# Kernel tuning notes

Measured on AMD Instinct MI355X. Metric: run time of the kernel, lower is better.

Reference implementation:

```python
import jax, jax.numpy as jnp
import numpy as np

DIM = 256
HALF = DIM // 2
B, S = 32, 4096
U_MAX = 4096          # upper bound on number of unique tree positions (positions < S)
MAX_DEPTH = 13        # bitlen(S) covers all path lengths for positions <= S


def setup_inputs() -> dict:
    key = jax.random.key(0)
    k1, k2, k3, k4, k5 = jax.random.split(key, 5)
    token_types = jax.random.randint(k1, (B, S), 0, 5, dtype=jnp.int32)
    node_positions = jax.random.randint(k2, (B, S), 0, S, dtype=jnp.int32)
    small_vals = jax.random.randint(k3, (B, S), 0, 4, dtype=jnp.int32)
    # deBruijn tokens (type 4) reference tree positions -> values must lie in unique(node_positions)
    token_values = jnp.where(token_types == 4, node_positions,
                   jnp.where(token_types == 3, -1, small_vals)).astype(jnp.int32)
    primitives = jax.random.normal(k4, (2, HALF, HALF), dtype=jnp.float32)
    identity = jnp.ones((1, HALF), dtype=jnp.float32)
    embed_weight = jax.random.normal(k5, (11, HALF), dtype=jnp.float32)
    return {"token_types": token_types, "token_values": token_values,
            "node_positions": node_positions, "primitives": primitives,
            "identity": identity, "embed_weight": embed_weight}


def cayley(X):
    # torch orthogonal(..., orthogonal_map='cayley'): A = tril(X) - tril(X)^T (skew), Q = (I - A/2)^{-1}(I + A/2)
    A = jnp.tril(X)
    A = A - jnp.swapaxes(A, -1, -2)
    I = jnp.eye(X.shape[-1], dtype=X.dtype)
    return jnp.linalg.solve(I - 0.5 * A, I + 0.5 * A)


def _forward(token_types, token_values, node_positions, primitives, identity, embed_weight):
    Q = cayley(primitives)                                   # [2, h, h] orthogonal maps
    flat_pos = node_positions.ravel()
    uniq, inv = jnp.unique(flat_pos, return_inverse=True, size=U_MAX, fill_value=S)
    inv = inv.ravel()

    # binary path of pos: bit d of pos for d < bitlen(pos)-1, padded with 2 (pos<=1 -> empty path)
    d = jnp.arange(MAX_DEPTH, dtype=uniq.dtype)
    bits = (uniq[:, None] >> d) & 1                           # [U, D]
    valid = (uniq[:, None] >> (d + 1)) > 0
    word = jnp.where(valid, bits, 2)                          # [U, D]

    maps0 = jnp.broadcast_to(identity, (U_MAX, HALF)).astype(primitives.dtype)

    def step(maps, b):                                        # maps [U, h], b [U]
        m0 = maps @ Q[0].T                                    # linear(maps, primitives[0])
        m1 = maps @ Q[1].T
        maps = jnp.where((b == 0)[:, None], m0,
                jnp.where((b == 1)[:, None], m1, maps))
        return maps, None

    path_emb, _ = jax.lax.scan(step, maps0, word.T)           # [U, h]

    pos_enc = path_emb[inv].reshape(B, S, HALF)               # positional encodings

    sos = token_types == 0
    bop = token_types == 1
    nop = token_types == 2
    oos = (token_types == 3) & (token_values == -1)
    db = token_types == 4

    emb_idx = jnp.where(bop, token_values + 1,
              jnp.where(nop, token_values + 5, 0))
    type_emb = embed_weight[emb_idx]                          # [B, S, h]

    db_idx = jnp.searchsorted(uniq, jnp.clip(token_values, 0, S - 1))  # bucketize into unique positions
    db_emb = path_emb[db_idx]                                 # [B, S, h]

    content = jnp.zeros_like(pos_enc)
    content = jnp.where(sos[..., None], embed_weight[0], content)
    content = jnp.where((bop | nop)[..., None], type_emb, content)
    content = jnp.where(db[..., None], db_emb, content)
    content = jnp.where(oos[..., None], embed_weight[10], content)

    return jnp.concatenate([content, pos_enc], axis=-1)       # [B, S, DIM]


def reference(token_types, token_values, node_positions, primitives, identity, embed_weight):
    return _forward(token_types, token_values, node_positions, primitives, identity, embed_weight)
```

## Files before the change

### kernel.cpp

```cpp
#include <hip/hip_runtime.h>

#define HALF 128
#define NMAT 16384
#define NTOK 131072

typedef float f4 __attribute__((ext_vector_type(4)));

__device__ __forceinline__ float nval(const float* __restrict__ X, int r, int c) {
    int mx = r > c ? r : c;
    int mn = r ^ c ^ mx;
    float x = X[mx * HALF + mn];
    return (r == c) ? 1.0f : (r > c ? 0.5f * x : -0.5f * x);
}


template<int S, bool FIRST>
__global__ __launch_bounds__(256) void k1_panel(const float* __restrict__ prim,
                                                const float* __restrict__ W,
                                                float* __restrict__ RBws) {
    __shared__ __align__(16) float Rs[16][132];
    __shared__ float Dc[16][17];
    const int b  = blockIdx.x;
    const int t  = threadIdx.x;
    const int k0 = S << 4;
    const float* __restrict__ X  = prim + b * NMAT;
    const float* __restrict__ Wb = W + b * NMAT;

    {
        const int j  = t >> 4;
        const int c0 = (t & 15) << 3;
        if (FIRST) {
            #pragma unroll
            for (int u = 0; u < 8; ++u) Rs[j][c0 + u] = nval(X, k0 + j, c0 + u);
        } else {
            float4 a  = *(const float4*)&Wb[(k0 + j) * HALF + c0];
            float4 b2 = *(const float4*)&Wb[(k0 + j) * HALF + c0 + 4];
            *(float4*)&Rs[j][c0]     = a;
            *(float4*)&Rs[j][c0 + 4] = b2;
        }
    }
    __syncthreads();

    if (t < 64) {
        const int cp = t & 15, q4 = t >> 4;
        float dd[4];
        #pragma unroll
        for (int i = 0; i < 4; ++i) dd[i] = Rs[q4 * 4 + i][k0 + cp];
        #pragma unroll
        for (int k = 0; k < 16; ++k) {
            float cv[4];
            #pragma unroll
            for (int i = 0; i < 4; ++i) cv[i] = __shfl(dd[i], (q4 << 4) | k);
            float rv   = __shfl(dd[k & 3], ((k >> 2) << 4) | cp);
            float dkk  = __shfl(rv, k);
            float dinv = 1.0f / dkk;
            float sv   = rv * dinv;
            bool  own  = (cp == k);
            float rf   = own ? dinv : sv;
            #pragma unroll
            for (int i = 0; i < 4; ++i)
                dd[i] = own ? (-dd[i] * dinv) : fmaf(-cv[i], sv, dd[i]);
            dd[k & 3] = (q4 == (k >> 2)) ? rf : dd[k & 3];
        }
        #pragma unroll
        for (int i = 0; i < 4; ++i) Dc[cp][q4 * 4 + i] = dd[i];
    }
    __syncthreads();

    {
        const int m  = t >> 4;
        const int c0 = (t & 15) << 3;
        float* __restrict__ RBb = RBws + b * (16 * HALF);
        if (c0 == k0 || c0 == k0 + 8) {
            #pragma unroll
            for (int u = 0; u < 8; ++u) RBb[m * HALF + c0 + u] = Dc[c0 + u - k0][m];
        } else {
            float acc[8] = {0.f,0.f,0.f,0.f,0.f,0.f,0.f,0.f};
            #pragma unroll
            for (int j = 0; j < 16; ++j) {
                float dj = Dc[j][m];
                #pragma unroll
                for (int u = 0; u < 8; ++u)
                    acc[u] = fmaf(dj, Rs[j][c0 + u], acc[u]);
            }
            *(float4*)&RBb[m * HALF + c0]     = make_float4(acc[0], acc[1], acc[2], acc[3]);
            *(float4*)&RBb[m * HALF + c0 + 4] = make_float4(acc[4], acc[5], acc[6], acc[7]);
        }
    }
}

template<int S, bool FIRST, bool LAST>
__global__ __launch_bounds__(256) void k1_update(const float* __restrict__ prim,
                                                 float* __restrict__ W,
                                                 const float* __restrict__ RBws) {
    __shared__ __align__(16) float RBs[16][132];
    __shared__ float Cs[16][17];
    const int blk = blockIdx.x;
    const int b   = blk >> 3;
    const int rg  = blk & 7;
    const int r0  = rg << 4;
    const int t   = threadIdx.x;
    const int k0  = S << 4;
    const float* __restrict__ X   = prim + b * NMAT;
    float* __restrict__ Wb        = W + b * NMAT;
    const float* __restrict__ RBb = RBws + b * (16 * HALF);

    {
        const int m  = t >> 4;
        const int c0 = (t & 15) << 3;
        *(float4*)&RBs[m][c0]     = *(const float4*)&RBb[m * HALF + c0];
        *(float4*)&RBs[m][c0 + 4] = *(const float4*)&RBb[m * HALF + c0 + 4];
    }
    {
        const int rr = t >> 4, m = t & 15;
        Cs[rr][m] = FIRST ? nval(X, r0 + rr, k0 + m)
                          : Wb[(r0 + rr) * HALF + k0 + m];
    }
    __syncthreads();

    const int rr = t >> 4;
    const int r  = r0 + rr;
    const int c0 = (t & 15) << 3;
    float w[8];

    if (rg == S) {
        #pragma unroll
        for (int u = 0; u < 8; ++u) w[u] = RBs[rr][c0 + u];
    } else {
        const bool pan = (c0 == k0) || (c0 == k0 + 8);
        if (pan) {
            #pragma unroll
            for (int u = 0; u < 8; ++u) w[u] = 0.0f;
        } else if (FIRST) {
            #pragma unroll
            for (int u = 0; u < 8; ++u) w[u] = nval(X, r, c0 + u);
        } else {
            float4 a  = *(const float4*)&Wb[r * HALF + c0];
            float4 b2 = *(const float4*)&Wb[r * HALF + c0 + 4];
            w[0]=a.x; w[1]=a.y; w[2]=a.z; w[3]=a.w;
            w[4]=b2.x; w[5]=b2.y; w[6]=b2.z; w[7]=b2.w;
        }
        #pragma unroll
        for (int m = 0; m < 16; ++m) {
            float cm = Cs[rr][m];
            #pragma unroll
            for (int u = 0; u < 8; ++u)
                w[u] = fmaf(-cm, RBs[m][c0 + u], w[u]);
        }
    }

    if (LAST) {
        #pragma unroll
        for (int u = 0; u < 8; ++u)
            w[u] = 2.0f * w[u] - ((r == c0 + u) ? 1.0f : 0.0f);
    }
    *(float4*)&Wb[r * HALF + c0]     = make_float4(w[0], w[1], w[2], w[3]);
    *(float4*)&Wb[r * HALF + c0 + 4] = make_float4(w[4], w[5], w[6], w[7]);
}

__global__ __launch_bounds__(256) void path_base(const float* __restrict__ QT,
                                                 const float* __restrict__ ident,
                                                 float* __restrict__ P) {
    __shared__ __align__(16) float vs[2][4][HALF];
    const int t    = threadIdx.x;
    const int rg   = t >> 6;
    const int jj   = (t & 63) << 1;
    const int v    = (blockIdx.x << 2) + rg;
    const int vmax = (blockIdx.x << 2) + 3;

    float2 cv = *(const float2*)&ident[jj];
    *(float2*)&vs[0][rg][jj] = cv;
    __syncthreads();

    int cur = 0;
    for (int d = 0; d < 8; ++d) {
        if ((vmax >> (d + 1)) == 0) break;
        const bool valid = (v >> (d + 1)) > 0;
        const float* __restrict__ Qm = QT + (((v >> d) & 1) ? NMAT : 0);
        float2 acc = make_float2(0.f, 0.f);
        #pragma unroll 4
        for (int cc = 0; cc < 128; cc += 4) {
            float4 v4 = *(const float4*)&vs[cur][rg][cc];
            float2 q0 = *(const float2*)&Qm[(cc+0)*HALF + jj];
            float2 q1 = *(const float2*)&Qm[(cc+1)*HALF + jj];
            float2 q2 = *(const float2*)&Qm[(cc+2)*HALF + jj];
            float2 q3 = *(const float2*)&Qm[(cc+3)*HALF + jj];
            acc.x = fmaf(v4.x,q0.x, fmaf(v4.y,q1.x, fmaf(v4.z,q2.x, fmaf(v4.w,q3.x, acc.x))));
            acc.y = fmaf(v4.x,q0.y, fmaf(v4.y,q1.y, fmaf(v4.z,q2.y, fmaf(v4.w,q3.y, acc.y))));
        }
        if (valid) cv = acc;
        *(float2*)&vs[cur ^ 1][rg][jj] = cv;
        __syncthreads();
        cur ^= 1;
    }
    *(float2*)&P[v * HALF + jj] = cv;
}

__global__ __launch_bounds__(256) void path_upper(const float* __restrict__ QT,
                                                  float* __restrict__ P) {
    __shared__ __align__(16) float vs[2][8][HALF];
    const int t  = threadIdx.x;
    const int j  = t & 127;
    const int h  = t >> 7;
    const int k  = 2 + (blockIdx.x >> 4);
    const int r0 = (blockIdx.x & 15) << 3;

    float acc[4];
    #pragma unroll
    for (int rr = 0; rr < 4; ++rr)
        acc[rr] = P[(128 + r0 + h * 4 + rr) * HALF + j];

    int p = 0;
    for (int d = 7; d < 13; ++d) {
        if ((k >> (d - 6)) == 0) break;
        const float* __restrict__ Qm = QT + (((k >> (d - 7)) & 1) ? NMAT : 0);
        #pragma unroll
        for (int rr = 0; rr < 4; ++rr) vs[p][h * 4 + rr][j] = acc[rr];
        __syncthreads();

        float nacc[4] = {0.f, 0.f, 0.f, 0.f};
        #pragma unroll 4
        for (int cc = 0; cc < 128; cc += 4) {
            float q0 = Qm[(cc + 0) * HALF + j];
            float q1 = Qm[(cc + 1) * HALF + j];
            float q2 = Qm[(cc + 2) * HALF + j];
            float q3 = Qm[(cc + 3) * HALF + j];
            #pragma unroll
            for (int rr = 0; rr < 4; ++rr) {
                float4 v4 = *(const float4*)&vs[p][h * 4 + rr][cc];
                nacc[rr] = fmaf(v4.x, q0,
                           fmaf(v4.y, q1,
                           fmaf(v4.z, q2,
                           fmaf(v4.w, q3, nacc[rr]))));
            }
        }
        #pragma unroll
        for (int rr = 0; rr < 4; ++rr) acc[rr] = nacc[rr];
        p ^= 1;
    }

    #pragma unroll
    for (int rr = 0; rr < 4; ++rr)
        P[((k << 7) | (r0 + h * 4 + rr)) * HALF + j] = acc[rr];
}

__global__ __launch_bounds__(256) void emit_out(const int* __restrict__ tt,
                                                const int* __restrict__ tv,
                                                const int* __restrict__ np,
                                                const float* __restrict__ P,
                                                const float* __restrict__ emb,
                                                float* __restrict__ out) {
    const int i  = (blockIdx.x << 2) + (threadIdx.x >> 6);
    const int jj = (threadIdx.x & 63) << 2;
    const int ty = tt[i];
    const int v  = tv[i];
    f4 val;
    if (jj < 128) {
        if (ty == 0)      val = *(const f4*)&emb[jj];
        else if (ty == 1) val = *(const f4*)&emb[(v + 1) * HALF + jj];
        else if (ty == 2) val = *(const f4*)&emb[(v + 5) * HALF + jj];
        else if (ty == 4) {
            int vc = v < 0 ? 0 : (v > 4095 ? 4095 : v);
            val = *(const f4*)&P[vc * HALF + jj];
        } else if (v == -1) val = *(const f4*)&emb[10 * HALF + jj];
        else { f4 z = {0.f, 0.f, 0.f, 0.f}; val = z; }
    } else {
        const int p = np[i];
        val = *(const f4*)&P[p * HALF + (jj - 128)];
    }
    __builtin_nontemporal_store(val, (f4*)&out[i * 256 + jj]);
}

extern "C" void kernel_launch(void* const* d_in, const int* in_sizes, int n_in,
                              void* d_out, int out_size, void* d_ws, size_t ws_size,
                              hipStream_t stream) {
    const int*   token_types = (const int*)  d_in[0];
    const int*   token_vals  = (const int*)  d_in[1];
    const int*   node_pos    = (const int*)  d_in[2];
    const float* prim        = (const float*)d_in[3];
    const float* ident       = (const float*)d_in[4];
    const float* emb         = (const float*)d_in[5];
    float* out = (float*)d_out;

    float* QT = (float*)d_ws;
    float* P  = (float*)((char*)d_ws + 262144);
    float* RB = (float*)((char*)d_ws + 2359296);

    k1_panel <0, true        ><<<2,  256, 0, stream>>>(prim, QT, RB);
    k1_update<0, true,  false><<<16, 256, 0, stream>>>(prim, QT, RB);
    k1_panel <1, false       ><<<2,  256, 0, stream>>>(prim, QT, RB);
    k1_update<1, false, false><<<16, 256, 0, stream>>>(prim, QT, RB);
    k1_panel <2, false       ><<<2,  256, 0, stream>>>(prim, QT, RB);
    k1_update<2, false, false><<<16, 256, 0, stream>>>(prim, QT, RB);
    k1_panel <3, false       ><<<2,  256, 0, stream>>>(prim, QT, RB);
    k1_update<3, false, false><<<16, 256, 0, stream>>>(prim, QT, RB);
    k1_panel <4, false       ><<<2,  256, 0, stream>>>(prim, QT, RB);
    k1_update<4, false, false><<<16, 256, 0, stream>>>(prim, QT, RB);
    k1_panel <5, false       ><<<2,  256, 0, stream>>>(prim, QT, RB);
    k1_update<5, false, false><<<16, 256, 0, stream>>>(prim, QT, RB);
    k1_panel <6, false       ><<<2,  256, 0, stream>>>(prim, QT, RB);
    k1_update<6, false, false><<<16, 256, 0, stream>>>(prim, QT, RB);
    k1_panel <7, false       ><<<2,  256, 0, stream>>>(prim, QT, RB);
    k1_update<7, false, true ><<<16, 256, 0, stream>>>(prim, QT, RB);

    path_base  <<<64,  256, 0, stream>>>(QT, ident, P);
    path_upper <<<480, 256, 0, stream>>>(QT, P);
    emit_out   <<<NTOK / 4, 256, 0, stream>>>(token_types, token_vals, node_pos,
                                              P, emb, out);
}
```

Baseline: 304.7 us.

## Fuse panel factorization and trailing update into one kernel per step

Each block-Gauss-Jordan step now recomputes the 16x16 panel inverse redundantly in every update block and keeps the panel row in shared memory, instead of writing it to global memory from a separate 2-block kernel. This halves the kernel launches in the Cayley solve, from 16 to 8. Matrices ping-pong between two workspace buffers so that blocks never read data another block is overwriting. The cost is redundant panel work in all 8 row-group blocks per matrix, plus extra shared memory.

```diff
diff --git a/kernel.cpp b/kernel.cpp
--- a/kernel.cpp
+++ b/kernel.cpp
@@ -13,18 +13,25 @@
     return (r == c) ? 1.0f : (r > c ? 0.5f * x : -0.5f * x);
 }
 
-
-template<int S, bool FIRST>
-__global__ __launch_bounds__(256) void k1_panel(const float* __restrict__ prim,
-                                                const float* __restrict__ W,
-                                                float* __restrict__ RBws) {
+template<bool FIRST, bool LAST>
+__global__ __launch_bounds__(256) void k1_step(const float* __restrict__ prim,
+                                               const float* __restrict__ Win,
+                                               float* __restrict__ Wout,
+                                               int S) {
     __shared__ __align__(16) float Rs[16][132];
     __shared__ float Dc[16][17];
-    const int b  = blockIdx.x;
-    const int t  = threadIdx.x;
-    const int k0 = S << 4;
+    __shared__ __align__(16) float RBs[16][132];
+    __shared__ float Cs[16][17];
+
+    const int blk = blockIdx.x;
+    const int b   = blk >> 3;
+    const int rg  = blk & 7;
+    const int r0  = rg << 4;
+    const int t   = threadIdx.x;
+    const int k0  = S << 4;
     const float* __restrict__ X  = prim + b * NMAT;
-    const float* __restrict__ Wb = W + b * NMAT;
+    const float* __restrict__ Wi = Win  + b * NMAT;
+    float*       __restrict__ Wo = Wout + b * NMAT;
 
     {
         const int j  = t >> 4;
@@ -33,11 +40,16 @@
             #pragma unroll
             for (int u = 0; u < 8; ++u) Rs[j][c0 + u] = nval(X, k0 + j, c0 + u);
         } else {
-            float4 a  = *(const float4*)&Wb[(k0 + j) * HALF + c0];
-            float4 b2 = *(const float4*)&Wb[(k0 + j) * HALF + c0 + 4];
+            float4 a  = *(const float4*)&Wi[(k0 + j) * HALF + c0];
+            float4 b2 = *(const float4*)&Wi[(k0 + j) * HALF + c0 + 4];
             *(float4*)&Rs[j][c0]     = a;
             *(float4*)&Rs[j][c0 + 4] = b2;
         }
+    }
+    {
+        const int rr = t >> 4, m = t & 15;
+        Cs[rr][m] = FIRST ? nval(X, r0 + rr, k0 + m)
+                          : Wi[(r0 + rr) * HALF + k0 + m];
     }
     __syncthreads();
 
@@ -70,10 +82,9 @@
     {
         const int m  = t >> 4;
         const int c0 = (t & 15) << 3;
-        float* __restrict__ RBb = RBws + b * (16 * HALF);
         if (c0 == k0 || c0 == k0 + 8) {
             #pragma unroll
-            for (int u = 0; u < 8; ++u) RBb[m * HALF + c0 + u] = Dc[c0 + u - k0][m];
+            for (int u = 0; u < 8; ++u) RBs[m][c0 + u] = Dc[c0 + u - k0][m];
         } else {
             float acc[8] = {0.f,0.f,0.f,0.f,0.f,0.f,0.f,0.f};
             #pragma unroll
@@ -83,79 +94,52 @@
                 for (int u = 0; u < 8; ++u)
                     acc[u] = fmaf(dj, Rs[j][c0 + u], acc[u]);
             }
-            *(float4*)&RBb[m * HALF + c0]     = make_float4(acc[0], acc[1], acc[2], acc[3]);
-            *(float4*)&RBb[m * HALF + c0 + 4] = make_float4(acc[4], acc[5], acc[6], acc[7]);
-        }
-    }
-}
-
-template<int S, bool FIRST, bool LAST>
-__global__ __launch_bounds__(256) void k1_update(const float* __restrict__ prim,
-                                                 float* __restrict__ W,
-                                                 const float* __restrict__ RBws) {
-    __shared__ __align__(16) float RBs[16][132];
-    __shared__ float Cs[16][17];
-    const int blk = blockIdx.x;
-    const int b   = blk >> 3;
-    const int rg  = blk & 7;
-    const int r0  = rg << 4;
-    const int t   = threadIdx.x;
-    const int k0  = S << 4;
-    const float* __restrict__ X   = prim + b * NMAT;
-    float* __restrict__ Wb        = W + b * NMAT;
-    const float* __restrict__ RBb = RBws + b * (16 * HALF);
-
-    {
-        const int m  = t >> 4;
+            *(float4*)&RBs[m][c0]     = make_float4(acc[0], acc[1], acc[2], acc[3]);
+            *(float4*)&RBs[m][c0 + 4] = make_float4(acc[4], acc[5], acc[6], acc[7]);
+        }
+    }
+    __syncthreads();
+
+    {
+        const int rr = t >> 4;
+        const int r  = r0 + rr;
         const int c0 = (t & 15) << 3;
-        *(float4*)&RBs[m][c0]     = *(const float4*)&RBb[m * HALF + c0];
-        *(float4*)&RBs[m][c0 + 4] = *(const float4*)&RBb[m * HALF + c0 + 4];
-    }
-    {
-        const int rr = t >> 4, m = t & 15;
-        Cs[rr][m] = FIRST ? nval(X, r0 + rr, k0 + m)
-                          : Wb[(r0 + rr) * HALF + k0 + m];
-    }
-    __syncthreads();
-
-    const int rr = t >> 4;
-    const int r  = r0 + rr;
-    const int c0 = (t & 15) << 3;
-    float w[8];
-
-    if (rg == S) {
-        #pragma unroll
-        for (int u = 0; u < 8; ++u) w[u] = RBs[rr][c0 + u];
-    } else {
-        const bool pan = (c0 == k0) || (c0 == k0 + 8);
-        if (pan) {
-            #pragma unroll
-            for (int u = 0; u < 8; ++u) w[u] = 0.0f;
-        } else if (FIRST) {
-            #pragma unroll
-            for (int u = 0; u < 8; ++u) w[u] = nval(X, r, c0 + u);
+        float w[8];
+
+        if (rg == S) {
+            #pragma unroll
+            for (int u = 0; u < 8; ++u) w[u] = RBs[rr][c0 + u];
         } else {
-            float4 a  = *(const float4*)&Wb[r * HALF + c0];
-            float4 b2 = *(const float4*)&Wb[r * HALF + c0 + 4];
-            w[0]=a.x; w[1]=a.y; w[2]=a.z; w[3]=a.w;
-            w[4]=b2.x; w[5]=b2.y; w[6]=b2.z; w[7]=b2.w;
-        }
-        #pragma unroll
-        for (int m = 0; m < 16; ++m) {
-            float cm = Cs[rr][m];
+            const bool pan = (c0 == k0) || (c0 == k0 + 8);
+            if (pan) {
+                #pragma unroll
+                for (int u = 0; u < 8; ++u) w[u] = 0.0f;
+            } else if (FIRST) {
+                #pragma unroll
+                for (int u = 0; u < 8; ++u) w[u] = nval(X, r, c0 + u);
+            } else {
+                float4 a  = *(const float4*)&Wi[r * HALF + c0];
+                float4 b2 = *(const float4*)&Wi[r * HALF + c0 + 4];
+                w[0]=a.x; w[1]=a.y; w[2]=a.z; w[3]=a.w;
+                w[4]=b2.x; w[5]=b2.y; w[6]=b2.z; w[7]=b2.w;
+            }
+            #pragma unroll
+            for (int m = 0; m < 16; ++m) {
+                float cm = Cs[rr][m];
+                #pragma unroll
+                for (int u = 0; u < 8; ++u)
+                    w[u] = fmaf(-cm, RBs[m][c0 + u], w[u]);
+            }
+        }
+
+        if (LAST) {
             #pragma unroll
             for (int u = 0; u < 8; ++u)
-                w[u] = fmaf(-cm, RBs[m][c0 + u], w[u]);
-        }
-    }
-
-    if (LAST) {
-        #pragma unroll
-        for (int u = 0; u < 8; ++u)
-            w[u] = 2.0f * w[u] - ((r == c0 + u) ? 1.0f : 0.0f);
-    }
-    *(float4*)&Wb[r * HALF + c0]     = make_float4(w[0], w[1], w[2], w[3]);
-    *(float4*)&Wb[r * HALF + c0 + 4] = make_float4(w[4], w[5], w[6], w[7]);
+                w[u] = 2.0f * w[u] - ((r == c0 + u) ? 1.0f : 0.0f);
+        }
+        *(float4*)&Wo[r * HALF + c0]     = make_float4(w[0], w[1], w[2], w[3]);
+        *(float4*)&Wo[r * HALF + c0 + 4] = make_float4(w[4], w[5], w[6], w[7]);
+    }
 }
 
 __global__ __launch_bounds__(256) void path_base(const float* __restrict__ QT,
@@ -284,24 +268,17 @@
 
     float* QT = (float*)d_ws;
     float* P  = (float*)((char*)d_ws + 262144);
-    float* RB = (float*)((char*)d_ws + 2359296);
-
-    k1_panel <0, true        ><<<2,  256, 0, stream>>>(prim, QT, RB);
-    k1_update<0, true,  false><<<16, 256, 0, stream>>>(prim, QT, RB);
-    k1_panel <1, false       ><<<2,  256, 0, stream>>>(prim, QT, RB);
-    k1_update<1, false, false><<<16, 256, 0, stream>>>(prim, QT, RB);
-    k1_panel <2, false       ><<<2,  256, 0, stream>>>(prim, QT, RB);
-    k1_update<2, false, false><<<16, 256, 0, stream>>>(prim, QT, RB);
-    k1_panel <3, false       ><<<2,  256, 0, stream>>>(prim, QT, RB);
-    k1_update<3, false, false><<<16, 256, 0, stream>>>(prim, QT, RB);
-    k1_panel <4, false       ><<<2,  256, 0, stream>>>(prim, QT, RB);
-    k1_update<4, false, false><<<16, 256, 0, stream>>>(prim, QT, RB);
-    k1_panel <5, false       ><<<2,  256, 0, stream>>>(prim, QT, RB);
-    k1_update<5, false, false><<<16, 256, 0, stream>>>(prim, QT, RB);
-    k1_panel <6, false       ><<<2,  256, 0, stream>>>(prim, QT, RB);
-    k1_update<6, false, false><<<16, 256, 0, stream>>>(prim, QT, RB);
-    k1_panel <7, false       ><<<2,  256, 0, stream>>>(prim, QT, RB);
-    k1_update<7, false, true ><<<16, 256, 0, stream>>>(prim, QT, RB);
+    float* W0 = (float*)((char*)d_ws + 262144);
+    float* W1 = (float*)((char*)d_ws + 262144 + 131072);
+
+    k1_step<true,  false><<<16, 256, 0, stream>>>(prim, W0, W0, 0);
+    k1_step<false, false><<<16, 256, 0, stream>>>(prim, W0, W1, 1);
+    k1_step<false, false><<<16, 256, 0, stream>>>(prim, W1, W0, 2);
+    k1_step<false, false><<<16, 256, 0, stream>>>(prim, W0, W1, 3);
+    k1_step<false, false><<<16, 256, 0, stream>>>(prim, W1, W0, 4);
+    k1_step<false, false><<<16, 256, 0, stream>>>(prim, W0, W1, 5);
+    k1_step<false, false><<<16, 256, 0, stream>>>(prim, W1, W0, 6);
+    k1_step<false, true ><<<16, 256, 0, stream>>>(prim, W0, QT, 7);
 
     path_base  <<<64,  256, 0, stream>>>(QT, ident, P);
     path_upper <<<480, 256, 0, stream>>>(QT, P);
```

After: 266.5 us, median of 2. -12.5%, faster.
